# Optimization experiments

Measured on AMD Instinct MI355X. Metric: run time of the kernel, lower is better.

Reference implementation:

```python
import jax, jax.numpy as jnp
import numpy as np

B, N, D = 4, 2048, 1024
H, DH = 16, 64
SCALE = DH ** -0.5


def setup_inputs() -> dict:
    key = jax.random.key(0)
    k1, k2, k3 = jax.random.split(key, 3)
    z = jax.random.normal(k1, (B, N, D), dtype=jnp.float32)
    w_qkv = jax.random.normal(k2, (D, 3 * H * DH), dtype=jnp.float32) * (D ** -0.5)
    w_out = jax.random.normal(k3, (H * DH, D), dtype=jnp.float32) * ((H * DH) ** -0.5)
    b_out = jnp.zeros((D,), dtype=jnp.float32)
    return {"z": z, "w_qkv": w_qkv, "w_out": w_out, "b_out": b_out}


def reference(z, w_qkv, w_out, b_out):
    # qkv projection: (B,N,D) @ (D,3*H*DH) -> split into q,k,v
    qkv = z @ w_qkv  # (B, N, 3*H*DH)
    q, k, v = jnp.split(qkv, 3, axis=-1)
    # (B, N, H*DH) -> (B, H, N, DH)
    def heads(t):
        return t.reshape(B, N, H, DH).transpose(0, 2, 1, 3)
    q, k, v = heads(q), heads(k), heads(v)
    # scaled dot-product attention with full NxN scores (matches original)
    dots = jnp.einsum('bhid,bhjd->bhij', q, k) * SCALE
    attn = jax.nn.softmax(dots, axis=-1)
    out = jnp.einsum('bhij,bhjd->bhid', attn, v)  # (B, H, N, DH)
    out = out.transpose(0, 2, 1, 3).reshape(B, N, H * DH)
    return out @ w_out + b_out  # dropout is identity in eval
```

## Files before the change

### kernel.cpp

```cpp
#include <hip/hip_runtime.h>
#include <hip/hip_bf16.h>
#include <cstdint>
#include <cstddef>

typedef __attribute__((ext_vector_type(8))) short short8;
typedef __attribute__((ext_vector_type(4))) float f32x4;
typedef __attribute__((ext_vector_type(4))) unsigned uint4v;

#define LDS_AS __attribute__((address_space(3)))
#define GLB_AS __attribute__((address_space(1)))

__device__ __forceinline__ unsigned short f32_bf16(float f) {
  unsigned u = __builtin_bit_cast(unsigned, f);
  u += 0x7fffu + ((u >> 16) & 1u);
  return (unsigned short)(u >> 16);
}

__device__ __forceinline__ unsigned cvt_pk_bf16(float lo, float hi) {
  unsigned r;
  asm("v_cvt_pk_bf16_f32 %0, %1, %2" : "=v"(r) : "v"(lo), "v"(hi));
  return r;
}

__global__ __launch_bounds__(256) void k_cvt(const float* __restrict__ in,
                                             unsigned short* __restrict__ out, int n4) {
  int i = blockIdx.x * 256 + threadIdx.x;
  if (i >= n4) return;
  float4 v = reinterpret_cast<const float4*>(in)[i];
  ushort4 o;
  o.x = f32_bf16(v.x); o.y = f32_bf16(v.y); o.z = f32_bf16(v.z); o.w = f32_bf16(v.w);
  reinterpret_cast<ushort4*>(out)[i] = o;
}

__global__ __launch_bounds__(256) void k_cvt_t2(const float* __restrict__ wq,
                                                unsigned short* __restrict__ oq,
                                                const float* __restrict__ wo,
                                                unsigned short* __restrict__ oo) {
  __shared__ float t[32][33];
  int bx = blockIdx.x;
  const float* in;
  unsigned short* out;
  int C;
  if (bx < 96) { in = wq; out = oq; C = 3072; }
  else         { in = wo; out = oo; C = 1024; bx -= 96; }
  const int R = 1024;
  int c0 = bx * 32, r0 = blockIdx.y * 32;
  int lr = threadIdx.x & 31, lw = threadIdx.x >> 5;
#pragma unroll
  for (int i = 0; i < 32; i += 8)
    t[lw + i][lr] = in[(size_t)(r0 + lw + i) * C + c0 + lr];
  __syncthreads();
#pragma unroll
  for (int i = 0; i < 32; i += 8)
    out[(size_t)(c0 + lw + i) * R + r0 + lr] = f32_bf16(t[lr][lw + i]);
}

__device__ __forceinline__ void gemm_bt_mainloop(
    const unsigned short* __restrict__ A, const unsigned short* __restrict__ Bt,
    int K, int m0, int n0, unsigned short* lds, int tid, f32x4 acc[4][4]) {
  const int w = tid >> 6, l = tid & 63;
  const int wr = w >> 1, wc = w & 1;
  const int lr = l & 15, lg = l >> 4;
  unsigned short* As = lds;
  unsigned short* Bs = lds + 8192;
  const int sslot = tid & 7;
  for (int kt = 0; kt < K; kt += 64) {
    __syncthreads();
#pragma unroll
    for (int i = 0; i < 4; ++i) {
      int idx = i * 256 + tid;
      int row = idx >> 3;
      int sw = sslot ^ (row & 7);
      __builtin_amdgcn_global_load_lds(
          (const GLB_AS unsigned int*)(A + (size_t)(m0 + row) * K + kt + sw * 8),
          (LDS_AS unsigned int*)(As + (size_t)idx * 8), 16, 0, 0);
    }
#pragma unroll
    for (int i = 0; i < 4; ++i) {
      int idx = i * 256 + tid;
      int row = idx >> 3;
      int sw = sslot ^ (row & 7);
      __builtin_amdgcn_global_load_lds(
          (const GLB_AS unsigned int*)(Bt + (size_t)(n0 + row) * K + kt + sw * 8),
          (LDS_AS unsigned int*)(Bs + (size_t)idx * 8), 16, 0, 0);
    }
    __syncthreads();
#pragma unroll
    for (int kc = 0; kc < 2; ++kc) {
      const int so = ((kc * 4 + lg) ^ (lr & 7)) * 8;
      short8 a[4], b[4];
#pragma unroll
      for (int m = 0; m < 4; ++m)
        a[m] = *reinterpret_cast<const short8*>(As + (wr * 64 + m * 16 + lr) * 64 + so);
#pragma unroll
      for (int n = 0; n < 4; ++n)
        b[n] = *reinterpret_cast<const short8*>(Bs + (wc * 64 + n * 16 + lr) * 64 + so);
      __builtin_amdgcn_s_setprio(1);
#pragma unroll
      for (int m = 0; m < 4; ++m)
#pragma unroll
        for (int n = 0; n < 4; ++n)
          acc[m][n] = __builtin_amdgcn_mfma_f32_16x16x32_bf16(a[m], b[n], acc[m][n], 0, 0, 0);
      __builtin_amdgcn_s_setprio(0);
    }
  }
}

__global__ __launch_bounds__(256) void k_gemm_qkv(
    const unsigned short* __restrict__ Zb, const unsigned short* __restrict__ Wt,
    unsigned short* __restrict__ Qb, unsigned short* __restrict__ Kb,
    unsigned short* __restrict__ Vt) {
  __shared__ unsigned short lds[16384];
  f32x4 acc[4][4];
#pragma unroll
  for (int m = 0; m < 4; ++m)
#pragma unroll
    for (int n = 0; n < 4; ++n) acc[m][n] = (f32x4){0.f, 0.f, 0.f, 0.f};
  const int m0 = blockIdx.x * 128, n0 = blockIdx.y * 128;
  gemm_bt_mainloop(Zb, Wt, 1024, m0, n0, lds, threadIdx.x, acc);
  const int tid = threadIdx.x, w = tid >> 6, l = tid & 63;
  const int wr = w >> 1, wc = w & 1, lr = l & 15, lg = l >> 4;
#pragma unroll
  for (int n = 0; n < 4; ++n) {
    int gc = n0 + wc * 64 + n * 16;
    int part = gc >> 10;
    int within = gc & 1023;
    int h = within >> 6;
    int dhb = (within & 63) + lr;
#pragma unroll
    for (int m = 0; m < 4; ++m) {
      int gr = m0 + wr * 64 + m * 16 + lg * 4;
      int b = gr >> 11, pos = gr & 2047;
      size_t bh = (size_t)(b * 16 + h);
      if (part == 0) {
        unsigned short* dst = Qb + bh * (2048 * 64) + (size_t)pos * 64 + dhb;
#pragma unroll
        for (int r = 0; r < 4; ++r) dst[r * 64] = f32_bf16(acc[m][n][r]);
      } else if (part == 1) {
        unsigned short* dst = Kb + bh * (2048 * 64) + (size_t)pos * 64 + dhb;
#pragma unroll
        for (int r = 0; r < 4; ++r) dst[r * 64] = f32_bf16(acc[m][n][r]);
      } else {
        unsigned short* dst = Vt + bh * (64 * 2048) + (size_t)dhb * 2048 + pos;
        ushort4 pv;
        pv.x = f32_bf16(acc[m][n][0]); pv.y = f32_bf16(acc[m][n][1]);
        pv.z = f32_bf16(acc[m][n][2]); pv.w = f32_bf16(acc[m][n][3]);
        *reinterpret_cast<ushort4*>(dst) = pv;
      }
    }
  }
}

__device__ __forceinline__ void softmax_pack(f32x4 s[4], float& m_r, float& l_r,
                                             f32x4 o[4], short8 pb[2], bool lgodd,
                                             float cc) {
  float t0 = fmaxf(fmaxf(s[0][0], s[0][1]), s[0][2]);
  float t1 = fmaxf(fmaxf(s[0][3], s[1][0]), s[1][1]);
  float t2 = fmaxf(fmaxf(s[1][2], s[1][3]), s[2][0]);
  float t3 = fmaxf(fmaxf(s[2][1], s[2][2]), s[2][3]);
  float t4 = fmaxf(fmaxf(s[3][0], s[3][1]), s[3][2]);
  float tl = fmaxf(fmaxf(fmaxf(t0, t1), fmaxf(t2, t3)), fmaxf(t4, s[3][3]));
  if (__any(tl > m_r + 8.0f)) {
    float tm = fmaxf(tl, __shfl_xor(tl, 16));
    tm = fmaxf(tm, __shfl_xor(tm, 32));
    float mn = fmaxf(m_r, tm);
    float al = __builtin_amdgcn_exp2f((m_r - mn) * cc);
    m_r = mn;
    l_r *= al;
#pragma unroll
    for (int c = 0; c < 4; ++c)
#pragma unroll
      for (int r = 0; r < 4; ++r) o[c][r] *= al;
  }
  float nb = m_r * cc;
  float rs = 0.f;
#pragma unroll
  for (int c = 0; c < 4; ++c)
#pragma unroll
    for (int r = 0; r < 4; ++r) {
      float p = __builtin_amdgcn_exp2f(s[c][r] * cc - nb);
      s[c][r] = p;
      rs += p;
    }
  rs += __shfl_xor(rs, 16);
  rs += __shfl_xor(rs, 32);
  l_r += rs;
  unsigned Ap[4], Bp[4];
#pragma unroll
  for (int c = 0; c < 4; ++c) {
    Ap[c] = cvt_pk_bf16(s[c][0], s[c][1]);
    Bp[c] = cvt_pk_bf16(s[c][2], s[c][3]);
  }
#pragma unroll
  for (int kc = 0; kc < 2; ++kc) {
    unsigned ua = Ap[2 * kc], va = Ap[2 * kc + 1];
    asm("v_permlane32_swap_b32 %0, %1" : "+v"(ua), "+v"(va));
    unsigned uas = (unsigned)__shfl_xor((int)ua, 16);
    unsigned vas = (unsigned)__shfl_xor((int)va, 16);
    unsigned w0 = lgodd ? vas : ua;
    unsigned w2 = lgodd ? va : uas;
    unsigned ub = Bp[2 * kc], vb = Bp[2 * kc + 1];
    asm("v_permlane32_swap_b32 %0, %1" : "+v"(ub), "+v"(vb));
    unsigned ubs = (unsigned)__shfl_xor((int)ub, 16);
    unsigned vbs = (unsigned)__shfl_xor((int)vb, 16);
    unsigned w1 = lgodd ? vbs : ub;
    unsigned w3 = lgodd ? vb : ubs;
    uint4v pw = (uint4v){w0, w1, w2, w3};
    pb[kc] = __builtin_bit_cast(short8, pw);
  }
}

__global__ __launch_bounds__(512, 4) void k_attn(
    const unsigned short* __restrict__ Q, const unsigned short* __restrict__ Kb,
    const unsigned short* __restrict__ Vt, unsigned short* __restrict__ O) {
  __shared__ unsigned short lds[16384];
  const int tid = threadIdx.x, w = tid >> 6, l = tid & 63;
  const int lr = l & 15, lg = l >> 4;
  const bool lgodd = (lg & 1) != 0;
  const int wg = blockIdx.x;
  const int xcd = wg & 7, local = wg >> 3;
  const int bh = xcd + ((local >> 3) << 3);
  const int qb = local & 7;
  const unsigned short* Qp = Q + (size_t)bh * (2048 * 64);
  const unsigned short* Kp = Kb + (size_t)bh * (2048 * 64);
  const unsigned short* Vp = Vt + (size_t)bh * (64 * 2048);
  const int q0 = qb * 256 + w * 32;

  short8 aq[2][2];
#pragma unroll
  for (int g = 0; g < 2; ++g)
#pragma unroll
    for (int kc = 0; kc < 2; ++kc)
      aq[g][kc] = *reinterpret_cast<const short8*>(
          Qp + (size_t)(q0 + g * 16 + lr) * 64 + kc * 32 + lg * 8);

  float m0r = -3e38f, l0r = 0.f, m1r = -3e38f, l1r = 0.f;
  f32x4 o0[4], o1[4];
#pragma unroll
  for (int c = 0; c < 4; ++c) {
    o0[c] = (f32x4){0.f, 0.f, 0.f, 0.f};
    o1[c] = (f32x4){0.f, 0.f, 0.f, 0.f};
  }
  const f32x4 zero4 = (f32x4){0.f, 0.f, 0.f, 0.f};
  const float cc = 0.125f * 1.44269504089f;

  const int so0 = (lg ^ (lr & 7)) * 8;
  const int so1 = ((4 + lg) ^ (lr & 7)) * 8;

  const int srow = tid >> 3, sslot = tid & 7;
  const int ssw = sslot ^ (srow & 7);
#define STAGE_KV(bufK, bufV, kv0)                                                     \
  {                                                                                   \
    __builtin_amdgcn_global_load_lds(                                                 \
        (const GLB_AS unsigned int*)(Kp + (size_t)((kv0) + srow) * 64 + ssw * 8),     \
        (LDS_AS unsigned int*)((bufK) + tid * 8), 16, 0, 0);                          \
    __builtin_amdgcn_global_load_lds(                                                 \
        (const GLB_AS unsigned int*)(Vp + (size_t)srow * 2048 + (kv0) + ssw * 8),     \
        (LDS_AS unsigned int*)((bufV) + tid * 8), 16, 0, 0);                          \
  }

  unsigned short* K0 = lds;
  unsigned short* V0 = lds + 4096;
  unsigned short* K1 = lds + 8192;
  unsigned short* V1 = lds + 12288;

  STAGE_KV(K0, V0, 0);
  __syncthreads();

  for (int t = 0; t < 32; ++t) {
    unsigned short* Ks = (t & 1) ? K1 : K0;
    unsigned short* Vs = (t & 1) ? V1 : V0;
    if (t < 31) {
      unsigned short* Kn = (t & 1) ? K0 : K1;
      unsigned short* Vn = (t & 1) ? V0 : V1;
      STAGE_KV(Kn, Vn, (t + 1) * 64);
    }
    f32x4 s0[4], s1[4];
    __builtin_amdgcn_s_setprio(1);
#pragma unroll
    for (int c = 0; c < 4; ++c) {
      const unsigned short* kb = Ks + c * 1024 + lr * 64;
      short8 ak0 = *reinterpret_cast<const short8*>(kb + so0);
      short8 ak1 = *reinterpret_cast<const short8*>(kb + so1);
      s0[c] = __builtin_amdgcn_mfma_f32_16x16x32_bf16(ak0, aq[0][0], zero4, 0, 0, 0);
      s1[c] = __builtin_amdgcn_mfma_f32_16x16x32_bf16(ak0, aq[1][0], zero4, 0, 0, 0);
      s0[c] = __builtin_amdgcn_mfma_f32_16x16x32_bf16(ak1, aq[0][1], s0[c], 0, 0, 0);
      s1[c] = __builtin_amdgcn_mfma_f32_16x16x32_bf16(ak1, aq[1][1], s1[c], 0, 0, 0);
    }
    __builtin_amdgcn_s_setprio(0);
    short8 pb0[2], pb1[2];
    softmax_pack(s0, m0r, l0r, o0, pb0, lgodd, cc);
    softmax_pack(s1, m1r, l1r, o1, pb1, lgodd, cc);
    __builtin_amdgcn_s_setprio(1);
#pragma unroll
    for (int c = 0; c < 4; ++c) {
      const unsigned short* vb = Vs + c * 1024 + lr * 64;
      short8 av0 = *reinterpret_cast<const short8*>(vb + so0);
      short8 av1 = *reinterpret_cast<const short8*>(vb + so1);
      o0[c] = __builtin_amdgcn_mfma_f32_16x16x32_bf16(av0, pb0[0], o0[c], 0, 0, 0);
      o1[c] = __builtin_amdgcn_mfma_f32_16x16x32_bf16(av0, pb1[0], o1[c], 0, 0, 0);
      o0[c] = __builtin_amdgcn_mfma_f32_16x16x32_bf16(av1, pb0[1], o0[c], 0, 0, 0);
      o1[c] = __builtin_amdgcn_mfma_f32_16x16x32_bf16(av1, pb1[1], o1[c], 0, 0, 0);
    }
    __builtin_amdgcn_s_setprio(0);
    __syncthreads();
  }

  const int b = bh >> 4, h = bh & 15;
#pragma unroll
  for (int g = 0; g < 2; ++g) {
    const float inv = 1.0f / (g ? l1r : l0r);
    const f32x4* o = g ? o1 : o0;
    const size_t row = (size_t)b * 2048 + q0 + g * 16 + lr;
#pragma unroll
    for (int c = 0; c < 4; ++c) {
      ushort4 pv;
      pv.x = f32_bf16(o[c][0] * inv);
      pv.y = f32_bf16(o[c][1] * inv);
      pv.z = f32_bf16(o[c][2] * inv);
      pv.w = f32_bf16(o[c][3] * inv);
      *reinterpret_cast<ushort4*>(const_cast<unsigned short*>(
          O + row * 1024 + h * 64 + c * 16 + lg * 4)) = pv;
    }
  }
#undef STAGE_KV
}

__global__ __launch_bounds__(256) void k_gemm_out(
    const unsigned short* __restrict__ Ob, const unsigned short* __restrict__ Wt,
    const float* __restrict__ bias, float* __restrict__ out) {
  __shared__ unsigned short lds[16384];
  f32x4 acc[4][4];
#pragma unroll
  for (int m = 0; m < 4; ++m)
#pragma unroll
    for (int n = 0; n < 4; ++n) acc[m][n] = (f32x4){0.f, 0.f, 0.f, 0.f};
  const int m0 = blockIdx.x * 128, n0 = blockIdx.y * 128;
  gemm_bt_mainloop(Ob, Wt, 1024, m0, n0, lds, threadIdx.x, acc);
  const int tid = threadIdx.x, w = tid >> 6, l = tid & 63;
  const int wr = w >> 1, wc = w & 1, lr = l & 15, lg = l >> 4;
#pragma unroll
  for (int n = 0; n < 4; ++n) {
    int gc = n0 + wc * 64 + n * 16 + lr;
    float bo = bias[gc];
#pragma unroll
    for (int m = 0; m < 4; ++m) {
      int gr = m0 + wr * 64 + m * 16 + lg * 4;
#pragma unroll
      for (int r = 0; r < 4; ++r)
        out[(size_t)(gr + r) * 1024 + gc] = acc[m][n][r] + bo;
    }
  }
}

extern "C" void kernel_launch(void* const* d_in, const int* in_sizes, int n_in,
                              void* d_out, int out_size, void* d_ws, size_t ws_size,
                              hipStream_t stream) {
  const float* z     = (const float*)d_in[0];
  const float* w_qkv = (const float*)d_in[1];
  const float* w_out = (const float*)d_in[2];
  const float* b_out = (const float*)d_in[3];
  float* out = (float*)d_out;

  unsigned short* ws = (unsigned short*)d_ws;
  unsigned short* Zb    = ws;
  unsigned short* Wqkvt = ws + 8388608;
  unsigned short* Woutt = ws + 11534336;
  unsigned short* Qb    = ws + 12582912;
  unsigned short* Kb    = ws + 20971520;
  unsigned short* Vt    = ws + 29360128;
  unsigned short* Ob    = Zb;

  k_cvt<<<dim3(8192), dim3(256), 0, stream>>>(z, Zb, 2097152);
  k_cvt_t2<<<dim3(128, 32), dim3(256), 0, stream>>>(w_qkv, Wqkvt, w_out, Woutt);
  k_gemm_qkv<<<dim3(64, 24), dim3(256), 0, stream>>>(Zb, Wqkvt, Qb, Kb, Vt);
  k_attn<<<dim3(512), dim3(512), 0, stream>>>(Qb, Kb, Vt, Ob);
  k_gemm_out<<<dim3(64, 8), dim3(256), 0, stream>>>(Ob, Woutt, b_out, out);
}
```

Measured before the change: 196.3 us.

## Shrink attention query tile to 16 rows per wave and double grid

Each wave now processes 16 query rows instead of 32, so a workgroup covers 128 queries and the attention grid doubles to 1024 blocks. This roughly halves accumulator and score registers and exposes more parallelism, at the cost of staging every K/V tile through LDS twice as often per query, which lowers arithmetic intensity. The softmax max, exp and sum reductions are also rewritten with vector elementwise operations, which may change the generated instructions.

Result: slower. 206.5 us (+5.2%).

```diff
diff --git a/kernel.cpp b/kernel.cpp
--- a/kernel.cpp
+++ b/kernel.cpp
@@ -154,12 +154,10 @@
 __device__ __forceinline__ void softmax_pack(f32x4 s[4], float& m_r, float& l_r,
                                              f32x4 o[4], short8 pb[2], bool lgodd,
                                              float cc) {
-  float t0 = fmaxf(fmaxf(s[0][0], s[0][1]), s[0][2]);
-  float t1 = fmaxf(fmaxf(s[0][3], s[1][0]), s[1][1]);
-  float t2 = fmaxf(fmaxf(s[1][2], s[1][3]), s[2][0]);
-  float t3 = fmaxf(fmaxf(s[2][1], s[2][2]), s[2][3]);
-  float t4 = fmaxf(fmaxf(s[3][0], s[3][1]), s[3][2]);
-  float tl = fmaxf(fmaxf(fmaxf(t0, t1), fmaxf(t2, t3)), fmaxf(t4, s[3][3]));
+  f32x4 m01 = __builtin_elementwise_max(s[0], s[1]);
+  f32x4 m23 = __builtin_elementwise_max(s[2], s[3]);
+  f32x4 m4 = __builtin_elementwise_max(m01, m23);
+  float tl = fmaxf(fmaxf(m4[0], m4[1]), fmaxf(m4[2], m4[3]));
   if (__any(tl > m_r + 8.0f)) {
     float tm = fmaxf(tl, __shfl_xor(tl, 16));
     tm = fmaxf(tm, __shfl_xor(tm, 32));
@@ -172,16 +170,17 @@
 #pragma unroll
       for (int r = 0; r < 4; ++r) o[c][r] *= al;
   }
-  float nb = m_r * cc;
-  float rs = 0.f;
-#pragma unroll
-  for (int c = 0; c < 4; ++c)
-#pragma unroll
-    for (int r = 0; r < 4; ++r) {
-      float p = __builtin_amdgcn_exp2f(s[c][r] * cc - nb);
-      s[c][r] = p;
-      rs += p;
-    }
+  const float nb = m_r * cc;
+  const f32x4 ccv = (f32x4){cc, cc, cc, cc};
+  const f32x4 nbv = (f32x4){nb, nb, nb, nb};
+#pragma unroll
+  for (int c = 0; c < 4; ++c) {
+    f32x4 t = s[c] * ccv - nbv;
+#pragma unroll
+    for (int r = 0; r < 4; ++r) s[c][r] = __builtin_amdgcn_exp2f(t[r]);
+  }
+  f32x4 sum4 = (s[0] + s[1]) + (s[2] + s[3]);
+  float rs = (sum4[0] + sum4[1]) + (sum4[2] + sum4[3]);
   rs += __shfl_xor(rs, 16);
   rs += __shfl_xor(rs, 32);
   l_r += rs;
@@ -219,28 +218,23 @@
   const bool lgodd = (lg & 1) != 0;
   const int wg = blockIdx.x;
   const int xcd = wg & 7, local = wg >> 3;
-  const int bh = xcd + ((local >> 3) << 3);
-  const int qb = local & 7;
+  const int bh = xcd + ((local >> 4) << 3);
+  const int qb = local & 15;
   const unsigned short* Qp = Q + (size_t)bh * (2048 * 64);
   const unsigned short* Kp = Kb + (size_t)bh * (2048 * 64);
   const unsigned short* Vp = Vt + (size_t)bh * (64 * 2048);
-  const int q0 = qb * 256 + w * 32;
-
-  short8 aq[2][2];
-#pragma unroll
-  for (int g = 0; g < 2; ++g)
-#pragma unroll
-    for (int kc = 0; kc < 2; ++kc)
-      aq[g][kc] = *reinterpret_cast<const short8*>(
-          Qp + (size_t)(q0 + g * 16 + lr) * 64 + kc * 32 + lg * 8);
-
-  float m0r = -3e38f, l0r = 0.f, m1r = -3e38f, l1r = 0.f;
-  f32x4 o0[4], o1[4];
-#pragma unroll
-  for (int c = 0; c < 4; ++c) {
-    o0[c] = (f32x4){0.f, 0.f, 0.f, 0.f};
-    o1[c] = (f32x4){0.f, 0.f, 0.f, 0.f};
-  }
+  const int q0 = qb * 128 + w * 16;
+
+  short8 aq[2];
+#pragma unroll
+  for (int kc = 0; kc < 2; ++kc)
+    aq[kc] = *reinterpret_cast<const short8*>(
+        Qp + (size_t)(q0 + lr) * 64 + kc * 32 + lg * 8);
+
+  float m_r = -3e38f, l_r = 0.f;
+  f32x4 o[4];
+#pragma unroll
+  for (int c = 0; c < 4; ++c) o[c] = (f32x4){0.f, 0.f, 0.f, 0.f};
   const f32x4 zero4 = (f32x4){0.f, 0.f, 0.f, 0.f};
   const float cc = 0.125f * 1.44269504089f;
 
@@ -275,53 +269,44 @@
       unsigned short* Vn = (t & 1) ? V0 : V1;
       STAGE_KV(Kn, Vn, (t + 1) * 64);
     }
-    f32x4 s0[4], s1[4];
+    f32x4 s[4];
     __builtin_amdgcn_s_setprio(1);
 #pragma unroll
     for (int c = 0; c < 4; ++c) {
       const unsigned short* kb = Ks + c * 1024 + lr * 64;
       short8 ak0 = *reinterpret_cast<const short8*>(kb + so0);
       short8 ak1 = *reinterpret_cast<const short8*>(kb + so1);
-      s0[c] = __builtin_amdgcn_mfma_f32_16x16x32_bf16(ak0, aq[0][0], zero4, 0, 0, 0);
-      s1[c] = __builtin_amdgcn_mfma_f32_16x16x32_bf16(ak0, aq[1][0], zero4, 0, 0, 0);
-      s0[c] = __builtin_amdgcn_mfma_f32_16x16x32_bf16(ak1, aq[0][1], s0[c], 0, 0, 0);
-      s1[c] = __builtin_amdgcn_mfma_f32_16x16x32_bf16(ak1, aq[1][1], s1[c], 0, 0, 0);
+      s[c] = __builtin_amdgcn_mfma_f32_16x16x32_bf16(ak0, aq[0], zero4, 0, 0, 0);
+      s[c] = __builtin_amdgcn_mfma_f32_16x16x32_bf16(ak1, aq[1], s[c], 0, 0, 0);
     }
     __builtin_amdgcn_s_setprio(0);
-    short8 pb0[2], pb1[2];
-    softmax_pack(s0, m0r, l0r, o0, pb0, lgodd, cc);
-    softmax_pack(s1, m1r, l1r, o1, pb1, lgodd, cc);
+    short8 pb[2];
+    softmax_pack(s, m_r, l_r, o, pb, lgodd, cc);
     __builtin_amdgcn_s_setprio(1);
 #pragma unroll
     for (int c = 0; c < 4; ++c) {
       const unsigned short* vb = Vs + c * 1024 + lr * 64;
       short8 av0 = *reinterpret_cast<const short8*>(vb + so0);
       short8 av1 = *reinterpret_cast<const short8*>(vb + so1);
-      o0[c] = __builtin_amdgcn_mfma_f32_16x16x32_bf16(av0, pb0[0], o0[c], 0, 0, 0);
-      o1[c] = __builtin_amdgcn_mfma_f32_16x16x32_bf16(av0, pb1[0], o1[c], 0, 0, 0);
-      o0[c] = __builtin_amdgcn_mfma_f32_16x16x32_bf16(av1, pb0[1], o0[c], 0, 0, 0);
-      o1[c] = __builtin_amdgcn_mfma_f32_16x16x32_bf16(av1, pb1[1], o1[c], 0, 0, 0);
+      o[c] = __builtin_amdgcn_mfma_f32_16x16x32_bf16(av0, pb[0], o[c], 0, 0, 0);
+      o[c] = __builtin_amdgcn_mfma_f32_16x16x32_bf16(av1, pb[1], o[c], 0, 0, 0);
     }
     __builtin_amdgcn_s_setprio(0);
     __syncthreads();
   }
 
   const int b = bh >> 4, h = bh & 15;
-#pragma unroll
-  for (int g = 0; g < 2; ++g) {
-    const float inv = 1.0f / (g ? l1r : l0r);
-    const f32x4* o = g ? o1 : o0;
-    const size_t row = (size_t)b * 2048 + q0 + g * 16 + lr;
-#pragma unroll
-    for (int c = 0; c < 4; ++c) {
-      ushort4 pv;
-      pv.x = f32_bf16(o[c][0] * inv);
-      pv.y = f32_bf16(o[c][1] * inv);
-      pv.z = f32_bf16(o[c][2] * inv);
-      pv.w = f32_bf16(o[c][3] * inv);
-      *reinterpret_cast<ushort4*>(const_cast<unsigned short*>(
-          O + row * 1024 + h * 64 + c * 16 + lg * 4)) = pv;
-    }
+  const float inv = 1.0f / l_r;
+  const size_t row = (size_t)b * 2048 + q0 + lr;
+#pragma unroll
+  for (int c = 0; c < 4; ++c) {
+    ushort4 pv;
+    pv.x = f32_bf16(o[c][0] * inv);
+    pv.y = f32_bf16(o[c][1] * inv);
+    pv.z = f32_bf16(o[c][2] * inv);
+    pv.w = f32_bf16(o[c][3] * inv);
+    *reinterpret_cast<ushort4*>(
+        const_cast<unsigned short*>(O + row * 1024 + h * 64 + c * 16 + lg * 4)) = pv;
   }
 #undef STAGE_KV
 }
@@ -374,6 +359,6 @@
   k_cvt<<<dim3(8192), dim3(256), 0, stream>>>(z, Zb, 2097152);
   k_cvt_t2<<<dim3(128, 32), dim3(256), 0, stream>>>(w_qkv, Wqkvt, w_out, Woutt);
   k_gemm_qkv<<<dim3(64, 24), dim3(256), 0, stream>>>(Zb, Wqkvt, Qb, Kb, Vt);
-  k_attn<<<dim3(512), dim3(512), 0, stream>>>(Qb, Kb, Vt, Ob);
+  k_attn<<<dim3(1024), dim3(512), 0, stream>>>(Qb, Kb, Vt, Ob);
   k_gemm_out<<<dim3(64, 8), dim3(256), 0, stream>>>(Ob, Woutt, b_out, out);
 }
```
